# Optimization experiments

Measured on AMD Instinct MI355X. Metric: run time of the kernel, lower is better.

The kernel has to match this reference:

```python
import jax, jax.numpy as jnp
import numpy as np

N_NODES = 100000


def gcn_conv(x, src, dst, W, b, n):
    # PyG GCNConv: x' = D^-1/2 (A + I) D^-1/2 (x W) + b
    h = x @ W  # [N, out] transform first (cheaper when out < in)
    loop = jnp.arange(n, dtype=src.dtype)
    s = jnp.concatenate([src, loop])
    d = jnp.concatenate([dst, loop])
    deg = jax.ops.segment_sum(jnp.ones_like(s, dtype=h.dtype), d, num_segments=n)
    dinv = jnp.where(deg > 0, jax.lax.rsqrt(deg), 0.0)
    norm = dinv[s] * dinv[d]  # [E+N]
    msg = h[s] * norm[:, None]  # [E+N, out]
    agg = jax.ops.segment_sum(msg, d, num_segments=n)
    return agg + b


def setup_inputs() -> dict:
    key = jax.random.key(0)
    ks = jax.random.split(key, 12)
    n, E, labels = N_NODES, 1600000, 128
    edges = jax.random.randint(ks[0], (2, E), 0, n, dtype=jnp.int64)
    features = jax.random.normal(ks[1], (n, labels), dtype=jnp.float32)

    def kaiming(k, fan_in, shape):
        return jax.random.normal(k, shape, dtype=jnp.float32) * np.sqrt(2.0 / fan_in)

    return {
        "edges": edges,
        "features": features,
        "W1": kaiming(ks[2], labels, (labels, 64)),
        "b1": jnp.zeros((64,), jnp.float32),
        "W2": kaiming(ks[3], 64, (64, 32)),
        "b2": jnp.zeros((32,), jnp.float32),
        "W3": kaiming(ks[4], 32, (32, 16)),
        "b3": jnp.zeros((16,), jnp.float32),
        "Wfc": kaiming(ks[5], 112, (112, 16)),
        "bfc": jnp.zeros((16,), jnp.float32),
    }


def reference(edges, features, W1, b1, W2, b2, W3, b3, Wfc, bfc):
    n = features.shape[0]
    src, dst = edges[0], edges[1]
    # eval mode: dropout is identity
    f1 = jax.nn.relu(gcn_conv(features, src, dst, W1, b1, n))  # [N, 64]
    f2 = jax.nn.relu(gcn_conv(f1, src, dst, W2, b2, n))        # [N, 32]
    f3 = jax.nn.relu(gcn_conv(f2, src, dst, W3, b3, n))        # [N, 16]
    cat = jnp.concatenate([f1, f2, f3], axis=1)                 # [N, 112]
    return jax.nn.relu(cat @ Wfc + bfc)                         # [N, 16]
```

## Files before the change

### kernel.cpp

```cpp
#include <hip/hip_runtime.h>

#define THREADS 256

typedef unsigned short u16;
typedef float f32x4 __attribute__((ext_vector_type(4)));
typedef short bf16x8 __attribute__((ext_vector_type(8)));

constexpr int SH = 9;
constexpr int NB = 1 << SH;
constexpr int TILE = 4096;

__device__ inline float bf2f(u16 u) {
  union { unsigned int i; float f; } c;
  c.i = ((unsigned int)u) << 16;
  return c.f;
}
__device__ inline u16 f2bf(float f) {
  union { float f; unsigned int i; } c;
  c.f = f;
  unsigned int r = c.i + 0x7fff + ((c.i >> 16) & 1);
  return (u16)(r >> 16);
}

union V8 {
  bf16x8 v;
  short s[8];
  u16 u[8];
};


__global__ void __launch_bounds__(256) k_hist(const int* __restrict__ dst,
                                              int* __restrict__ ghist, int E,
                                              int nblk, int nbk) {
  __shared__ int lcnt[NB];
  int t = threadIdx.x, blk = blockIdx.x;
  for (int i = t; i < nbk; i += 256) lcnt[i] = 0;
  __syncthreads();
  int beg = blk * TILE, end = min(beg + TILE, E);
  for (int e = beg + t; e < end; e += 256) atomicAdd(&lcnt[dst[e] >> SH], 1);
  __syncthreads();
  for (int i = t; i < nbk; i += 256) ghist[i * nblk + blk] = lcnt[i];
}

__global__ void __launch_bounds__(256) k_scanA(int* __restrict__ ghist,
                                               int* __restrict__ bsum, int nblk) {
  __shared__ int sc[256];
  int i = blockIdx.x, t = threadIdx.x;
  int* row = ghist + (size_t)i * nblk;
  int e0 = 2 * t, e1 = 2 * t + 1;
  int a0 = (e0 < nblk) ? row[e0] : 0;
  int a1 = (e1 < nblk) ? row[e1] : 0;
  int s = a0 + a1;
  sc[t] = s;
  __syncthreads();
  for (int o = 1; o < 256; o <<= 1) {
    int x = (t >= o) ? sc[t - o] : 0;
    __syncthreads();
    sc[t] += x;
    __syncthreads();
  }
  int base = sc[t] - s;
  if (e0 < nblk) row[e0] = base;
  if (e1 < nblk) row[e1] = base + a0;
  if (t == 255) bsum[i] = sc[255];
}

__global__ void __launch_bounds__(256) k_part(const int* __restrict__ src,
                                              const int* __restrict__ dst,
                                              const int* __restrict__ goff,
                                              const int* __restrict__ bsum,
                                              int* __restrict__ ebuf, int E,
                                              int nblk, int nbk) {
  __shared__ int lcur[NB];
  __shared__ int sb[256];
  int t = threadIdx.x, blk = blockIdx.x;
  int v = (t < nbk) ? bsum[t] : 0;
  sb[t] = v;
  __syncthreads();
  for (int o = 1; o < 256; o <<= 1) {
    int x = (t >= o) ? sb[t - o] : 0;
    __syncthreads();
    sb[t] += x;
    __syncthreads();
  }
  for (int i = t; i < nbk; i += 256)
    lcur[i] = goff[(size_t)i * nblk + blk] + (i ? sb[i - 1] : 0);
  __syncthreads();
  int beg = blk * TILE, end = min(beg + TILE, E);
  for (int e = beg + t; e < end; e += 256) {
    int s = src[e], d = dst[e];
    int p = atomicAdd(&lcur[d >> SH], 1);
    ebuf[p] = s | ((d & (NB - 1)) << 20);
  }
}

__global__ void __launch_bounds__(256) k_refine(
    const int* __restrict__ ebuf, const int* __restrict__ goff,
    const int* __restrict__ bsum, int* __restrict__ rowptr,
    int* __restrict__ colsrc, float* __restrict__ dinv,
    int n, int nbk, int nblk, int E) {
  __shared__ int cnt[NB];
  __shared__ int cur[NB];
  __shared__ int sc[256];
  __shared__ int bex[256];
  int b = blockIdx.x, t = threadIdx.x;
  {
    int v = (t < nbk) ? bsum[t] : 0;
    bex[t] = v;
    __syncthreads();
    for (int o = 1; o < 256; o <<= 1) {
      int x = (t >= o) ? bex[t - o] : 0;
      __syncthreads();
      bex[t] += x;
      __syncthreads();
    }
  }
  int beg = goff[(size_t)b * nblk] + (b ? bex[b - 1] : 0);
  int end = (b + 1 < nbk) ? goff[(size_t)(b + 1) * nblk] + bex[b] : E;
  cnt[t] = 0;
  cnt[t + 256] = 0;
  __syncthreads();
  for (int i = beg + t; i < end; i += 256) atomicAdd(&cnt[ebuf[i] >> 20], 1);
  __syncthreads();
  int c0 = cnt[2 * t], c1 = cnt[2 * t + 1];
  int a = c0 + c1;
  sc[t] = a;
  __syncthreads();
  for (int o = 1; o < 256; o <<= 1) {
    int x = (t >= o) ? sc[t - o] : 0;
    __syncthreads();
    sc[t] += x;
    __syncthreads();
  }
  int base0 = beg + sc[t] - a;
  int base1 = base0 + c0;
  int node0 = b << SH;
  int n0 = node0 + 2 * t, n1 = n0 + 1;
  cur[2 * t] = base0;
  cur[2 * t + 1] = base1;
  if (n0 <= n) rowptr[n0] = base0;
  if (n1 <= n) rowptr[n1] = base1;
  if (n0 < n) dinv[n0] = rsqrtf((float)(c0 + 1));
  if (n1 < n) dinv[n1] = rsqrtf((float)(c1 + 1));
  if (b == nbk - 1 && t == 0) rowptr[n] = E;
  __syncthreads();
  for (int i = beg + t; i < end; i += 256) {
    int w = ebuf[i];
    int p = atomicAdd(&cur[w >> 20], 1);
    colsrc[p] = w & 0xFFFFF;
  }
}


template <int KC, int FOUT, bool BF16IN>
__global__ void __launch_bounds__(256) k_xform(
    const void* __restrict__ xin, const float* __restrict__ Wg,
    const float* __restrict__ dinv, u16* __restrict__ g, int n) {
  constexpr int FIN = KC * 32;
  constexpr int NC = FOUT / 16;
  constexpr int ASLOTS = 8 * KC * 64;
  constexpr int WSLOTS = KC * NC * 64;
  __shared__ short xa[ASLOTS * 8];
  __shared__ short wb[WSLOTS * 8];

  int t = threadIdx.x;
  int r0 = blockIdx.x * 128;

  for (int s = t; s < WSLOTS; s += 256) {
    int lane = s & 63, q = s >> 6;
    int nc = q % NC, kc = q / NC;
    int col = nc * 16 + (lane & 15);
    int kr = kc * 32 + (lane >> 4) * 8;
    V8 v;
#pragma unroll
    for (int j = 0; j < 8; ++j) v.s[j] = (short)f2bf(Wg[(kr + j) * FOUT + col]);
    *(bf16x8*)&wb[s * 8] = v.v;
  }

  for (int s = t; s < ASLOTS; s += 256) {
    int lane = s & 63, q = s >> 6;
    int kc = q % KC, mtile = q / KC;
    int row = mtile * 16 + (lane & 15);
    int k = kc * 32 + (lane >> 4) * 8;
    int gr = r0 + row;
    V8 v;
    if (gr < n) {
      if constexpr (BF16IN) {
        v.v = *(const bf16x8*)((const u16*)xin + (size_t)gr * FIN + k);
      } else {
        const float* xf = (const float*)xin + (size_t)gr * FIN + k;
        float4 p = *(const float4*)xf;
        float4 q4 = *(const float4*)(xf + 4);
        v.s[0] = (short)f2bf(p.x); v.s[1] = (short)f2bf(p.y);
        v.s[2] = (short)f2bf(p.z); v.s[3] = (short)f2bf(p.w);
        v.s[4] = (short)f2bf(q4.x); v.s[5] = (short)f2bf(q4.y);
        v.s[6] = (short)f2bf(q4.z); v.s[7] = (short)f2bf(q4.w);
      }
    } else {
      for (int j = 0; j < 8; ++j) v.s[j] = 0;
    }
    *(bf16x8*)&xa[s * 8] = v.v;
  }
  __syncthreads();

  int ln = t & 63, wv = t >> 6;
  int m0 = wv * 2;

  bf16x8 bf[KC * NC];
#pragma unroll
  for (int i = 0; i < KC * NC; ++i) bf[i] = *(const bf16x8*)&wb[(i * 64 + ln) * 8];

  f32x4 acc[2][NC];
#pragma unroll
  for (int i = 0; i < 2; ++i)
#pragma unroll
    for (int j = 0; j < NC; ++j) acc[i][j] = {0.f, 0.f, 0.f, 0.f};

#pragma unroll
  for (int kc = 0; kc < KC; ++kc) {
    bf16x8 a0 = *(const bf16x8*)&xa[(((m0 + 0) * KC + kc) * 64 + ln) * 8];
    bf16x8 a1 = *(const bf16x8*)&xa[(((m0 + 1) * KC + kc) * 64 + ln) * 8];
#pragma unroll
    for (int nc = 0; nc < NC; ++nc) {
      acc[0][nc] = __builtin_amdgcn_mfma_f32_16x16x32_bf16(a0, bf[kc * NC + nc], acc[0][nc], 0, 0, 0);
      acc[1][nc] = __builtin_amdgcn_mfma_f32_16x16x32_bf16(a1, bf[kc * NC + nc], acc[1][nc], 0, 0, 0);
    }
  }

  int colb = ln & 15, rq = ln >> 4;
#pragma unroll
  for (int mt2 = 0; mt2 < 2; ++mt2) {
#pragma unroll
    for (int reg = 0; reg < 4; ++reg) {
      int gr = r0 + (m0 + mt2) * 16 + rq * 4 + reg;
      if (gr < n) {
        float di = dinv[gr];
#pragma unroll
        for (int nc = 0; nc < NC; ++nc)
          g[(size_t)gr * FOUT + nc * 16 + colb] = f2bf(acc[mt2][nc][reg] * di);
      }
    }
  }
}


template <int GF, int GOUT, int FCROW0, int FCROWS, int MODE>
__global__ void __launch_bounds__(256) k_gx(
    const u16* __restrict__ gin, const int* __restrict__ rowptr,
    const int* __restrict__ colsrc, const float* __restrict__ dinv,
    const float* __restrict__ bias, const float* __restrict__ Wg,
    const float* __restrict__ Wfc, const float* __restrict__ bfc,
    u16* __restrict__ gout, float* __restrict__ out, int n) {
  constexpr int KC = (GF + 31) / 32;
  constexpr int NCG = (GOUT > 0) ? (GOUT / 16) : 1;
  constexpr int ASLOTS = 8 * KC * 64;
  constexpr int WGSLOTS = (GOUT > 0) ? (KC * NCG * 64) : 64;
  constexpr int WFSLOTS = KC * 64;
  __shared__ short xa[ASLOTS * 8];
  __shared__ short wgb[WGSLOTS * 8];
  __shared__ short wfb[WFSLOTS * 8];

  int t = threadIdx.x;
  int r0 = blockIdx.x * 128;

  {
    V8 z;
#pragma unroll
    for (int j = 0; j < 8; ++j) z.s[j] = 0;
    for (int s = t; s < ASLOTS; s += 256) *(bf16x8*)&xa[s * 8] = z.v;
  }
  if constexpr (GOUT > 0) {
    for (int s = t; s < WGSLOTS; s += 256) {
      int lane = s & 63, q = s >> 6;
      int nc = q % NCG, kc = q / NCG;
      int col = nc * 16 + (lane & 15);
      int kr = kc * 32 + (lane >> 4) * 8;
      V8 v;
#pragma unroll
      for (int j = 0; j < 8; ++j) v.s[j] = (short)f2bf(Wg[(kr + j) * GOUT + col]);
      *(bf16x8*)&wgb[s * 8] = v.v;
    }
  }
  for (int s = t; s < WFSLOTS; s += 256) {
    int lane = s & 63, kc = s >> 6;
    int col = lane & 15;
    int kr = kc * 32 + (lane >> 4) * 8;
    V8 v;
#pragma unroll
    for (int j = 0; j < 8; ++j)
      v.s[j] = (kr + j < FCROWS) ? (short)f2bf(Wfc[(FCROW0 + kr + j) * 16 + col]) : (short)0;
    *(bf16x8*)&wfb[s * 8] = v.v;
  }
  __syncthreads();

  {
    constexpr int LPG = GF / 8;
    constexpr int NPW = 64 / LPG;
    constexpr int PASSES = 128 / (NPW * 4);
    int ln = t & 63, wib = t >> 6;
    int lanein = ln % LPG, grp = ln / LPG;
    int f0 = lanein * 8;
    float bb[8];
#pragma unroll
    for (int j = 0; j < 8; ++j) bb[j] = bias[f0 + j];
#pragma unroll
    for (int pass = 0; pass < PASSES; ++pass) {
      int lr = pass * (NPW * 4) + wib * NPW + grp;
      int gr = r0 + lr;
      if (gr < n) {
        int b = rowptr[gr], e = rowptr[gr + 1];
        float p0[8], p1[8], p2[8], p3[8];
        {
          V8 u;
          u.v = *(const bf16x8*)&gin[(size_t)gr * GF + f0];
#pragma unroll
          for (int j = 0; j < 8; ++j) {
            p0[j] = bf2f(u.u[j]);
            p1[j] = 0.f; p2[j] = 0.f; p3[j] = 0.f;
          }
        }
        int i = b;
        for (; i + 4 <= e; i += 4) {
          int s0 = colsrc[i + 0], s1 = colsrc[i + 1];
          int s2 = colsrc[i + 2], s3 = colsrc[i + 3];
          V8 u0, u1, u2, u3;
          u0.v = *(const bf16x8*)&gin[(size_t)s0 * GF + f0];
          u1.v = *(const bf16x8*)&gin[(size_t)s1 * GF + f0];
          u2.v = *(const bf16x8*)&gin[(size_t)s2 * GF + f0];
          u3.v = *(const bf16x8*)&gin[(size_t)s3 * GF + f0];
#pragma unroll
          for (int j = 0; j < 8; ++j) {
            p0[j] += bf2f(u0.u[j]);
            p1[j] += bf2f(u1.u[j]);
            p2[j] += bf2f(u2.u[j]);
            p3[j] += bf2f(u3.u[j]);
          }
        }
        for (; i < e; ++i) {
          int s = colsrc[i];
          V8 u;
          u.v = *(const bf16x8*)&gin[(size_t)s * GF + f0];
#pragma unroll
          for (int j = 0; j < 8; ++j) p1[j] += bf2f(u.u[j]);
        }
        float di = dinv[gr];
        V8 o;
#pragma unroll
        for (int j = 0; j < 8; ++j) {
          float a = (p0[j] + p1[j]) + (p2[j] + p3[j]);
          o.u[j] = f2bf(fmaxf(fmaf(a, di, bb[j]), 0.f));
        }
        int kc = f0 >> 5, q = (f0 >> 3) & 3;
        int slot = ((lr >> 4) * KC + kc) * 64 + ((lr & 15) | (q << 4));
        *(bf16x8*)&xa[slot * 8] = o.v;
      }
    }
  }
  __syncthreads();

  int ln = t & 63, wv = t >> 6;
  int m0 = wv * 2;

  bf16x8 wgf[KC * NCG];
  if constexpr (GOUT > 0) {
#pragma unroll
    for (int i = 0; i < KC * NCG; ++i) wgf[i] = *(const bf16x8*)&wgb[(i * 64 + ln) * 8];
  }
  bf16x8 wff[KC];
#pragma unroll
  for (int i = 0; i < KC; ++i) wff[i] = *(const bf16x8*)&wfb[(i * 64 + ln) * 8];

  f32x4 accG[2][NCG];
  f32x4 accF[2];
#pragma unroll
  for (int i = 0; i < 2; ++i) {
    accF[i] = {0.f, 0.f, 0.f, 0.f};
#pragma unroll
    for (int j = 0; j < NCG; ++j) accG[i][j] = {0.f, 0.f, 0.f, 0.f};
  }

#pragma unroll
  for (int kc = 0; kc < KC; ++kc) {
    bf16x8 a0 = *(const bf16x8*)&xa[(((m0 + 0) * KC + kc) * 64 + ln) * 8];
    bf16x8 a1 = *(const bf16x8*)&xa[(((m0 + 1) * KC + kc) * 64 + ln) * 8];
    if constexpr (GOUT > 0) {
#pragma unroll
      for (int nc = 0; nc < NCG; ++nc) {
        accG[0][nc] = __builtin_amdgcn_mfma_f32_16x16x32_bf16(a0, wgf[kc * NCG + nc], accG[0][nc], 0, 0, 0);
        accG[1][nc] = __builtin_amdgcn_mfma_f32_16x16x32_bf16(a1, wgf[kc * NCG + nc], accG[1][nc], 0, 0, 0);
      }
    }
    accF[0] = __builtin_amdgcn_mfma_f32_16x16x32_bf16(a0, wff[kc], accF[0], 0, 0, 0);
    accF[1] = __builtin_amdgcn_mfma_f32_16x16x32_bf16(a1, wff[kc], accF[1], 0, 0, 0);
  }

  int colb = ln & 15, rq = ln >> 4;
#pragma unroll
  for (int mt2 = 0; mt2 < 2; ++mt2) {
#pragma unroll
    for (int reg = 0; reg < 4; ++reg) {
      int gr = r0 + (m0 + mt2) * 16 + rq * 4 + reg;
      if (gr < n) {
        if constexpr (GOUT > 0) {
          float di = dinv[gr];
#pragma unroll
          for (int nc = 0; nc < NCG; ++nc)
            gout[(size_t)gr * GOUT + nc * 16 + colb] = f2bf(accG[mt2][nc][reg] * di);
        }
        float fcv = accF[mt2][reg];
        size_t oi = (size_t)gr * 16 + colb;
        if constexpr (MODE == 0) {
          out[oi] = fcv;
        } else if constexpr (MODE == 1) {
          out[oi] += fcv;
        } else {
          out[oi] = fmaxf(out[oi] + fcv + bfc[colb], 0.f);
        }
      }
    }
  }
}


extern "C" void kernel_launch(void* const* d_in, const int* in_sizes, int n_in,
                              void* d_out, int out_size, void* d_ws, size_t ws_size,
                              hipStream_t stream) {
  const int* edges = (const int*)d_in[0];
  const float* feat = (const float*)d_in[1];
  const float* W1 = (const float*)d_in[2];
  const float* b1 = (const float*)d_in[3];
  const float* W2 = (const float*)d_in[4];
  const float* b2 = (const float*)d_in[5];
  const float* W3 = (const float*)d_in[6];
  const float* b3 = (const float*)d_in[7];
  const float* Wfc = (const float*)d_in[8];
  const float* bfc = (const float*)d_in[9];
  float* out = (float*)d_out;

  const int E = in_sizes[0] / 2;
  const int n = in_sizes[1] / 128;
  const int* srcp = edges;
  const int* dstp = edges + E;
  const int nbk = (n + NB - 1) >> SH;
  const int nblk = (E + TILE - 1) / TILE;

  char* w = (char*)d_ws;
  auto carve = [&](size_t bytes) {
    void* p = (void*)w;
    w += (bytes + 255) & ~(size_t)255;
    return p;
  };
  int* ghist = (int*)carve((size_t)nbk * nblk * 4);
  int* bsum = (int*)carve(256 * 4);
  int* rowptr = (int*)carve(((size_t)n + 1) * 4);
  float* dinv = (float*)carve((size_t)n * 4);
  int* colsrc = (int*)carve((size_t)E * 4);
  size_t big = (size_t)E * 4 > (size_t)n * 128 ? (size_t)E * 4 : (size_t)n * 128;
  void* shared_big = carve(big);
  int* ebuf = (int*)shared_big;
  u16* g1 = (u16*)shared_big;
  u16* g3 = (u16*)shared_big;
  u16* g2 = (u16*)carve((size_t)n * 32 * 2);

  k_hist<<<nblk, 256, 0, stream>>>(dstp, ghist, E, nblk, nbk);
  k_scanA<<<nbk, 256, 0, stream>>>(ghist, bsum, nblk);
  k_part<<<nblk, 256, 0, stream>>>(srcp, dstp, ghist, bsum, ebuf, E, nblk, nbk);
  k_refine<<<nbk, 256, 0, stream>>>(ebuf, ghist, bsum, rowptr, colsrc, dinv, n, nbk, nblk, E);

  const int xb = (n + 127) / 128;

  k_xform<4, 64, false><<<xb, 256, 0, stream>>>(feat, W1, dinv, g1, n);
  k_gx<64, 32, 0, 64, 0><<<xb, 256, 0, stream>>>(
      g1, rowptr, colsrc, dinv, b1, W2, Wfc, bfc, g2, out, n);
  k_gx<32, 16, 64, 32, 1><<<xb, 256, 0, stream>>>(
      g2, rowptr, colsrc, dinv, b2, W3, Wfc, bfc, g3, out, n);
  k_gx<16, 0, 96, 16, 2><<<xb, 256, 0, stream>>>(
      g3, rowptr, colsrc, dinv, b3, (const float*)nullptr, Wfc, bfc,
      (u16*)nullptr, out, n);
}
```

Measured before the change: 157.6 us.

## Split fused gather+GEMM kernels into grid-stride gather and separate MFMA transform

Replaces each fused gather-plus-GEMM kernel with two kernels. The first is a grid-stride gather that writes the activated features to memory in bf16. The second is a transform kernel that applies the next layer's weight and the FC slice with MFMA. The last layer uses a dedicated gather+FC kernel that moves gathered rows into MFMA operand layout with ds_bpermute instead of LDS. The aim is to decouple the latency-bound irregular gather from the LDS-heavy GEMM, improving occupancy and load balance. The cost is extra kernel launches and extra intermediate round trips through global memory.

```diff
diff --git a/kernel.cpp b/kernel.cpp
--- a/kernel.cpp
+++ b/kernel.cpp
@@ -1,6 +1,4 @@
 #include <hip/hip_runtime.h>
-
-#define THREADS 256
 
 typedef unsigned short u16;
 typedef float f32x4 __attribute__((ext_vector_type(4)));
@@ -26,6 +24,7 @@
   bf16x8 v;
   short s[8];
   u16 u[8];
+  int i[4];
 };
 
 
@@ -152,16 +151,19 @@
 }
 
 
-template <int KC, int FOUT, bool BF16IN>
+template <int KC, int FOUT, bool BF16IN, int FCROW0, int FCROWS, int MODE>
 __global__ void __launch_bounds__(256) k_xform(
     const void* __restrict__ xin, const float* __restrict__ Wg,
-    const float* __restrict__ dinv, u16* __restrict__ g, int n) {
+    const float* __restrict__ dinv, u16* __restrict__ g,
+    const float* __restrict__ Wfc, float* __restrict__ out, int n) {
   constexpr int FIN = KC * 32;
   constexpr int NC = FOUT / 16;
   constexpr int ASLOTS = 8 * KC * 64;
   constexpr int WSLOTS = KC * NC * 64;
+  constexpr int WFS = (FCROWS > 0) ? KC * 64 : 1;
   __shared__ short xa[ASLOTS * 8];
   __shared__ short wb[WSLOTS * 8];
+  __shared__ short wfb[WFS * 8];
 
   int t = threadIdx.x;
   int r0 = blockIdx.x * 128;
@@ -175,6 +177,18 @@
 #pragma unroll
     for (int j = 0; j < 8; ++j) v.s[j] = (short)f2bf(Wg[(kr + j) * FOUT + col]);
     *(bf16x8*)&wb[s * 8] = v.v;
+  }
+  if constexpr (FCROWS > 0) {
+    for (int s = t; s < WFS; s += 256) {
+      int lane = s & 63, kc = s >> 6;
+      int col = lane & 15;
+      int kr = kc * 32 + (lane >> 4) * 8;
+      V8 v;
+#pragma unroll
+      for (int j = 0; j < 8; ++j)
+        v.s[j] = (kr + j < FCROWS) ? (short)f2bf(Wfc[(FCROW0 + kr + j) * 16 + col]) : (short)0;
+      *(bf16x8*)&wfb[s * 8] = v.v;
+    }
   }
 
   for (int s = t; s < ASLOTS; s += 256) {
@@ -209,12 +223,20 @@
   bf16x8 bf[KC * NC];
 #pragma unroll
   for (int i = 0; i < KC * NC; ++i) bf[i] = *(const bf16x8*)&wb[(i * 64 + ln) * 8];
+  bf16x8 wff[(FCROWS > 0) ? KC : 1];
+  if constexpr (FCROWS > 0) {
+#pragma unroll
+    for (int i = 0; i < KC; ++i) wff[i] = *(const bf16x8*)&wfb[(i * 64 + ln) * 8];
+  }
 
   f32x4 acc[2][NC];
-#pragma unroll
-  for (int i = 0; i < 2; ++i)
+  f32x4 accF[2];
+#pragma unroll
+  for (int i = 0; i < 2; ++i) {
+    accF[i] = {0.f, 0.f, 0.f, 0.f};
 #pragma unroll
     for (int j = 0; j < NC; ++j) acc[i][j] = {0.f, 0.f, 0.f, 0.f};
+  }
 
 #pragma unroll
   for (int kc = 0; kc < KC; ++kc) {
@@ -224,6 +246,10 @@
     for (int nc = 0; nc < NC; ++nc) {
       acc[0][nc] = __builtin_amdgcn_mfma_f32_16x16x32_bf16(a0, bf[kc * NC + nc], acc[0][nc], 0, 0, 0);
       acc[1][nc] = __builtin_amdgcn_mfma_f32_16x16x32_bf16(a1, bf[kc * NC + nc], acc[1][nc], 0, 0, 0);
+    }
+    if constexpr (FCROWS > 0) {
+      accF[0] = __builtin_amdgcn_mfma_f32_16x16x32_bf16(a0, wff[kc], accF[0], 0, 0, 0);
+      accF[1] = __builtin_amdgcn_mfma_f32_16x16x32_bf16(a1, wff[kc], accF[1], 0, 0, 0);
     }
   }
 
@@ -238,183 +264,183 @@
 #pragma unroll
         for (int nc = 0; nc < NC; ++nc)
           g[(size_t)gr * FOUT + nc * 16 + colb] = f2bf(acc[mt2][nc][reg] * di);
-      }
-    }
-  }
-}
-
-
-template <int GF, int GOUT, int FCROW0, int FCROWS, int MODE>
-__global__ void __launch_bounds__(256) k_gx(
-    const u16* __restrict__ gin, const int* __restrict__ rowptr,
+        if constexpr (FCROWS > 0) {
+          size_t oi = (size_t)gr * 16 + colb;
+          if constexpr (MODE == 0) out[oi] = accF[mt2][reg];
+          else out[oi] += accF[mt2][reg];
+        }
+      }
+    }
+  }
+}
+
+
+template <int F>
+__global__ void __launch_bounds__(256) k_gather_fin(
+    const u16* __restrict__ g, const int* __restrict__ rowptr,
     const int* __restrict__ colsrc, const float* __restrict__ dinv,
-    const float* __restrict__ bias, const float* __restrict__ Wg,
-    const float* __restrict__ Wfc, const float* __restrict__ bfc,
-    u16* __restrict__ gout, float* __restrict__ out, int n) {
-  constexpr int KC = (GF + 31) / 32;
-  constexpr int NCG = (GOUT > 0) ? (GOUT / 16) : 1;
-  constexpr int ASLOTS = 8 * KC * 64;
-  constexpr int WGSLOTS = (GOUT > 0) ? (KC * NCG * 64) : 64;
-  constexpr int WFSLOTS = KC * 64;
-  __shared__ short xa[ASLOTS * 8];
-  __shared__ short wgb[WGSLOTS * 8];
-  __shared__ short wfb[WFSLOTS * 8];
-
+    const float* __restrict__ bias, u16* __restrict__ fout, int n) {
+  constexpr int LPG = F / 8;
+  constexpr int G = 64 / LPG;
   int t = threadIdx.x;
-  int r0 = blockIdx.x * 128;
-
-  {
-    V8 z;
-#pragma unroll
-    for (int j = 0; j < 8; ++j) z.s[j] = 0;
-    for (int s = t; s < ASLOTS; s += 256) *(bf16x8*)&xa[s * 8] = z.v;
-  }
-  if constexpr (GOUT > 0) {
-    for (int s = t; s < WGSLOTS; s += 256) {
-      int lane = s & 63, q = s >> 6;
-      int nc = q % NCG, kc = q / NCG;
-      int col = nc * 16 + (lane & 15);
-      int kr = kc * 32 + (lane >> 4) * 8;
-      V8 v;
-#pragma unroll
-      for (int j = 0; j < 8; ++j) v.s[j] = (short)f2bf(Wg[(kr + j) * GOUT + col]);
-      *(bf16x8*)&wgb[s * 8] = v.v;
-    }
-  }
-  for (int s = t; s < WFSLOTS; s += 256) {
-    int lane = s & 63, kc = s >> 6;
+  int ln = t & 63, wib = t >> 6;
+  int lanein = ln % LPG, grp = ln / LPG;
+  int f0 = lanein * 8;
+  float bb[8];
+#pragma unroll
+  for (int j = 0; j < 8; ++j) bb[j] = bias[f0 + j];
+  int gw = blockIdx.x * (blockDim.x >> 6) + wib;
+  int nwaves = (gridDim.x * blockDim.x) >> 6;
+  for (int node = gw * G + grp; node < n; node += nwaves * G) {
+    int b = rowptr[node], e = rowptr[node + 1];
+    float p0[8], p1[8], p2[8], p3[8];
+    {
+      V8 u;
+      u.v = *(const bf16x8*)&g[(size_t)node * F + f0];
+#pragma unroll
+      for (int j = 0; j < 8; ++j) {
+        p0[j] = bf2f(u.u[j]);
+        p1[j] = 0.f; p2[j] = 0.f; p3[j] = 0.f;
+      }
+    }
+    int i = b;
+    for (; i + 4 <= e; i += 4) {
+      int s0 = colsrc[i + 0], s1 = colsrc[i + 1];
+      int s2 = colsrc[i + 2], s3 = colsrc[i + 3];
+      V8 u0, u1, u2, u3;
+      u0.v = *(const bf16x8*)&g[(size_t)s0 * F + f0];
+      u1.v = *(const bf16x8*)&g[(size_t)s1 * F + f0];
+      u2.v = *(const bf16x8*)&g[(size_t)s2 * F + f0];
+      u3.v = *(const bf16x8*)&g[(size_t)s3 * F + f0];
+#pragma unroll
+      for (int j = 0; j < 8; ++j) {
+        p0[j] += bf2f(u0.u[j]);
+        p1[j] += bf2f(u1.u[j]);
+        p2[j] += bf2f(u2.u[j]);
+        p3[j] += bf2f(u3.u[j]);
+      }
+    }
+    for (; i < e; ++i) {
+      int s = colsrc[i];
+      V8 u;
+      u.v = *(const bf16x8*)&g[(size_t)s * F + f0];
+#pragma unroll
+      for (int j = 0; j < 8; ++j) p1[j] += bf2f(u.u[j]);
+    }
+    float di = dinv[node];
+    V8 o;
+#pragma unroll
+    for (int j = 0; j < 8; ++j) {
+      float a = (p0[j] + p1[j]) + (p2[j] + p3[j]);
+      o.u[j] = f2bf(fmaxf(fmaf(a, di, bb[j]), 0.f));
+    }
+    *(bf16x8*)&fout[(size_t)node * F + f0] = o.v;
+  }
+}
+
+
+__global__ void __launch_bounds__(256) k_gather_fc(
+    const u16* __restrict__ g3, const int* __restrict__ rowptr,
+    const int* __restrict__ colsrc, const float* __restrict__ dinv,
+    const float* __restrict__ b3, const float* __restrict__ Wfc,
+    const float* __restrict__ bfc, float* __restrict__ out, int n) {
+  __shared__ short wfb[64 * 8];
+  int t = threadIdx.x;
+  for (int s = t; s < 64; s += 256) {
+    int lane = s & 63;
     int col = lane & 15;
-    int kr = kc * 32 + (lane >> 4) * 8;
+    int kr = (lane >> 4) * 8;
     V8 v;
 #pragma unroll
     for (int j = 0; j < 8; ++j)
-      v.s[j] = (kr + j < FCROWS) ? (short)f2bf(Wfc[(FCROW0 + kr + j) * 16 + col]) : (short)0;
+      v.s[j] = (kr + j < 16) ? (short)f2bf(Wfc[(96 + kr + j) * 16 + col]) : (short)0;
     *(bf16x8*)&wfb[s * 8] = v.v;
   }
   __syncthreads();
 
-  {
-    constexpr int LPG = GF / 8;
-    constexpr int NPW = 64 / LPG;
-    constexpr int PASSES = 128 / (NPW * 4);
-    int ln = t & 63, wib = t >> 6;
-    int lanein = ln % LPG, grp = ln / LPG;
-    int f0 = lanein * 8;
-    float bb[8];
-#pragma unroll
-    for (int j = 0; j < 8; ++j) bb[j] = bias[f0 + j];
-#pragma unroll
-    for (int pass = 0; pass < PASSES; ++pass) {
-      int lr = pass * (NPW * 4) + wib * NPW + grp;
-      int gr = r0 + lr;
-      if (gr < n) {
-        int b = rowptr[gr], e = rowptr[gr + 1];
-        float p0[8], p1[8], p2[8], p3[8];
-        {
-          V8 u;
-          u.v = *(const bf16x8*)&gin[(size_t)gr * GF + f0];
-#pragma unroll
-          for (int j = 0; j < 8; ++j) {
-            p0[j] = bf2f(u.u[j]);
-            p1[j] = 0.f; p2[j] = 0.f; p3[j] = 0.f;
-          }
+  int ln = t & 63, wv = t >> 6;
+  bf16x8 wff = *(const bf16x8*)&wfb[ln * 8];
+  int lanein = ln & 1, grp = ln >> 1;
+  int f0 = lanein * 8;
+  float bb[8];
+#pragma unroll
+  for (int j = 0; j < 8; ++j) bb[j] = b3[f0 + j];
+  int colb = ln & 15, rq = ln >> 4, kq = ln >> 4;
+  float bfcc = bfc[colb];
+
+  int wid = blockIdx.x * 4 + wv;
+  int nw = gridDim.x * 4;
+  int nch = (n + 31) / 32;
+
+  for (int ch = wid; ch < nch; ch += nw) {
+    int gr = ch * 32 + grp;
+    V8 o;
+    if (gr < n) {
+      int b = rowptr[gr], e = rowptr[gr + 1];
+      float p0[8], p1[8], p2[8], p3[8];
+      {
+        V8 u;
+        u.v = *(const bf16x8*)&g3[(size_t)gr * 16 + f0];
+#pragma unroll
+        for (int j = 0; j < 8; ++j) {
+          p0[j] = bf2f(u.u[j]);
+          p1[j] = 0.f; p2[j] = 0.f; p3[j] = 0.f;
         }
-        int i = b;
-        for (; i + 4 <= e; i += 4) {
-          int s0 = colsrc[i + 0], s1 = colsrc[i + 1];
-          int s2 = colsrc[i + 2], s3 = colsrc[i + 3];
-          V8 u0, u1, u2, u3;
-          u0.v = *(const bf16x8*)&gin[(size_t)s0 * GF + f0];
-          u1.v = *(const bf16x8*)&gin[(size_t)s1 * GF + f0];
-          u2.v = *(const bf16x8*)&gin[(size_t)s2 * GF + f0];
-          u3.v = *(const bf16x8*)&gin[(size_t)s3 * GF + f0];
-#pragma unroll
-          for (int j = 0; j < 8; ++j) {
-            p0[j] += bf2f(u0.u[j]);
-            p1[j] += bf2f(u1.u[j]);
-            p2[j] += bf2f(u2.u[j]);
-            p3[j] += bf2f(u3.u[j]);
-          }
+      }
+      int i = b;
+      for (; i + 4 <= e; i += 4) {
+        int s0 = colsrc[i + 0], s1 = colsrc[i + 1];
+        int s2 = colsrc[i + 2], s3 = colsrc[i + 3];
+        V8 u0, u1, u2, u3;
+        u0.v = *(const bf16x8*)&g3[(size_t)s0 * 16 + f0];
+        u1.v = *(const bf16x8*)&g3[(size_t)s1 * 16 + f0];
+        u2.v = *(const bf16x8*)&g3[(size_t)s2 * 16 + f0];
+        u3.v = *(const bf16x8*)&g3[(size_t)s3 * 16 + f0];
+#pragma unroll
+        for (int j = 0; j < 8; ++j) {
+          p0[j] += bf2f(u0.u[j]);
+          p1[j] += bf2f(u1.u[j]);
+          p2[j] += bf2f(u2.u[j]);
+          p3[j] += bf2f(u3.u[j]);
         }
-        for (; i < e; ++i) {
-          int s = colsrc[i];
-          V8 u;
-          u.v = *(const bf16x8*)&gin[(size_t)s * GF + f0];
-#pragma unroll
-          for (int j = 0; j < 8; ++j) p1[j] += bf2f(u.u[j]);
-        }
-        float di = dinv[gr];
-        V8 o;
-#pragma unroll
-        for (int j = 0; j < 8; ++j) {
-          float a = (p0[j] + p1[j]) + (p2[j] + p3[j]);
-          o.u[j] = f2bf(fmaxf(fmaf(a, di, bb[j]), 0.f));
-        }
-        int kc = f0 >> 5, q = (f0 >> 3) & 3;
-        int slot = ((lr >> 4) * KC + kc) * 64 + ((lr & 15) | (q << 4));
-        *(bf16x8*)&xa[slot * 8] = o.v;
-      }
-    }
-  }
-  __syncthreads();
-
-  int ln = t & 63, wv = t >> 6;
-  int m0 = wv * 2;
-
-  bf16x8 wgf[KC * NCG];
-  if constexpr (GOUT > 0) {
-#pragma unroll
-    for (int i = 0; i < KC * NCG; ++i) wgf[i] = *(const bf16x8*)&wgb[(i * 64 + ln) * 8];
-  }
-  bf16x8 wff[KC];
-#pragma unroll
-  for (int i = 0; i < KC; ++i) wff[i] = *(const bf16x8*)&wfb[(i * 64 + ln) * 8];
-
-  f32x4 accG[2][NCG];
-  f32x4 accF[2];
-#pragma unroll
-  for (int i = 0; i < 2; ++i) {
-    accF[i] = {0.f, 0.f, 0.f, 0.f};
-#pragma unroll
-    for (int j = 0; j < NCG; ++j) accG[i][j] = {0.f, 0.f, 0.f, 0.f};
-  }
-
-#pragma unroll
-  for (int kc = 0; kc < KC; ++kc) {
-    bf16x8 a0 = *(const bf16x8*)&xa[(((m0 + 0) * KC + kc) * 64 + ln) * 8];
-    bf16x8 a1 = *(const bf16x8*)&xa[(((m0 + 1) * KC + kc) * 64 + ln) * 8];
-    if constexpr (GOUT > 0) {
-#pragma unroll
-      for (int nc = 0; nc < NCG; ++nc) {
-        accG[0][nc] = __builtin_amdgcn_mfma_f32_16x16x32_bf16(a0, wgf[kc * NCG + nc], accG[0][nc], 0, 0, 0);
-        accG[1][nc] = __builtin_amdgcn_mfma_f32_16x16x32_bf16(a1, wgf[kc * NCG + nc], accG[1][nc], 0, 0, 0);
-      }
-    }
-    accF[0] = __builtin_amdgcn_mfma_f32_16x16x32_bf16(a0, wff[kc], accF[0], 0, 0, 0);
-    accF[1] = __builtin_amdgcn_mfma_f32_16x16x32_bf16(a1, wff[kc], accF[1], 0, 0, 0);
-  }
-
-  int colb = ln & 15, rq = ln >> 4;
-#pragma unroll
-  for (int mt2 = 0; mt2 < 2; ++mt2) {
-#pragma unroll
-    for (int reg = 0; reg < 4; ++reg) {
-      int gr = r0 + (m0 + mt2) * 16 + rq * 4 + reg;
-      if (gr < n) {
-        if constexpr (GOUT > 0) {
-          float di = dinv[gr];
-#pragma unroll
-          for (int nc = 0; nc < NCG; ++nc)
-            gout[(size_t)gr * GOUT + nc * 16 + colb] = f2bf(accG[mt2][nc][reg] * di);
-        }
-        float fcv = accF[mt2][reg];
-        size_t oi = (size_t)gr * 16 + colb;
-        if constexpr (MODE == 0) {
-          out[oi] = fcv;
-        } else if constexpr (MODE == 1) {
-          out[oi] += fcv;
-        } else {
-          out[oi] = fmaxf(out[oi] + fcv + bfc[colb], 0.f);
+      }
+      for (; i < e; ++i) {
+        int s = colsrc[i];
+        V8 u;
+        u.v = *(const bf16x8*)&g3[(size_t)s * 16 + f0];
+#pragma unroll
+        for (int j = 0; j < 8; ++j) p1[j] += bf2f(u.u[j]);
+      }
+      float di = dinv[gr];
+#pragma unroll
+      for (int j = 0; j < 8; ++j) {
+        float a = (p0[j] + p1[j]) + (p2[j] + p3[j]);
+        o.u[j] = f2bf(fmaxf(fmaf(a, di, bb[j]), 0.f));
+      }
+    } else {
+#pragma unroll
+      for (int j = 0; j < 8; ++j) o.s[j] = 0;
+    }
+
+#pragma unroll
+    for (int tt = 0; tt < 2; ++tt) {
+      int sl4 = (((ln & 15) + tt * 16) * 2 + (kq & 1)) * 4;
+      V8 A;
+#pragma unroll
+      for (int d = 0; d < 4; ++d)
+        A.i[d] = __builtin_amdgcn_ds_bpermute(sl4, o.i[d]);
+      if (kq >= 2) {
+#pragma unroll
+        for (int j = 0; j < 8; ++j) A.s[j] = 0;
+      }
+      f32x4 acc = {0.f, 0.f, 0.f, 0.f};
+      acc = __builtin_amdgcn_mfma_f32_16x16x32_bf16(A.v, wff, acc, 0, 0, 0);
+#pragma unroll
+      for (int reg = 0; reg < 4; ++reg) {
+        int go = ch * 32 + tt * 16 + rq * 4 + reg;
+        if (go < n) {
+          size_t oi = (size_t)go * 16 + colb;
+          out[oi] = fmaxf(out[oi] + acc[reg] + bfcc, 0.f);
         }
       }
     }
@@ -455,12 +481,15 @@
   int* rowptr = (int*)carve(((size_t)n + 1) * 4);
   float* dinv = (float*)carve((size_t)n * 4);
   int* colsrc = (int*)carve((size_t)E * 4);
-  size_t big = (size_t)E * 4 > (size_t)n * 128 ? (size_t)E * 4 : (size_t)n * 128;
-  void* shared_big = carve(big);
-  int* ebuf = (int*)shared_big;
-  u16* g1 = (u16*)shared_big;
-  u16* g3 = (u16*)shared_big;
-  u16* g2 = (u16*)carve((size_t)n * 32 * 2);
+  size_t bigA = (size_t)E * 4 > (size_t)n * 128 ? (size_t)E * 4 : (size_t)n * 128;
+  void* pA = carve(bigA);
+  int* ebuf = (int*)pA;
+  u16* g1 = (u16*)pA;
+  u16* f2 = (u16*)pA;
+  void* pB = carve((size_t)n * 128);
+  u16* f1 = (u16*)pB;
+  u16* g3 = (u16*)pB;
+  u16* g2 = (u16*)carve((size_t)n * 64);
 
   k_hist<<<nblk, 256, 0, stream>>>(dstp, ghist, E, nblk, nbk);
   k_scanA<<<nbk, 256, 0, stream>>>(ghist, bsum, nblk);
@@ -469,12 +498,13 @@
 
   const int xb = (n + 127) / 128;
 
-  k_xform<4, 64, false><<<xb, 256, 0, stream>>>(feat, W1, dinv, g1, n);
-  k_gx<64, 32, 0, 64, 0><<<xb, 256, 0, stream>>>(
-      g1, rowptr, colsrc, dinv, b1, W2, Wfc, bfc, g2, out, n);
-  k_gx<32, 16, 64, 32, 1><<<xb, 256, 0, stream>>>(
-      g2, rowptr, colsrc, dinv, b2, W3, Wfc, bfc, g3, out, n);
-  k_gx<16, 0, 96, 16, 2><<<xb, 256, 0, stream>>>(
-      g3, rowptr, colsrc, dinv, b3, (const float*)nullptr, Wfc, bfc,
-      (u16*)nullptr, out, n);
-}
+  k_xform<4, 64, false, 0, 0, 0><<<xb, 256, 0, stream>>>(
+      feat, W1, dinv, g1, (const float*)nullptr, (float*)nullptr, n);
+  k_gather_fin<64><<<2048, 256, 0, stream>>>(g1, rowptr, colsrc, dinv, b1, f1, n);
+  k_xform<2, 32, true, 0, 64, 0><<<xb, 256, 0, stream>>>(
+      f1, W2, dinv, g2, Wfc, out, n);
+  k_gather_fin<32><<<2048, 256, 0, stream>>>(g2, rowptr, colsrc, dinv, b2, f2, n);
+  k_xform<1, 16, true, 64, 32, 1><<<xb, 256, 0, stream>>>(
+      f2, W3, dinv, g3, Wfc, out, n);
+  k_gather_fc<<<xb, 256, 0, stream>>>(g3, rowptr, colsrc, dinv, b3, Wfc, bfc, out, n);
+}
```

After: 164.3 us. 4.3% more time.
